# Kernel optimization log

Hardware: AMD Instinct MI355X
Metric: run time of the kernel (lower is better)

## Reference

```python
import jax, jax.numpy as jnp
import numpy as np

B, N, D, M, H = 16, 196, 512, 20, 8


def setup_inputs() -> dict:
    key = jax.random.key(0)
    ks = jax.random.split(key, 8)
    s = 0.02  # small init scale for stable activations
    return {
        "F_clean": jax.random.normal(ks[0], (B, N, D), dtype=jnp.float32),
        "in_proj_w": jax.random.normal(ks[1], (3 * D, D), dtype=jnp.float32) * s,
        "in_proj_b": jnp.zeros((3 * D,), jnp.float32),
        "out_w": jax.random.normal(ks[2], (D, D), dtype=jnp.float32) * s,
        "out_b": jnp.zeros((D,), jnp.float32),
        "w1": jax.random.normal(ks[3], (D, D), dtype=jnp.float32) * s,
        "b1": jnp.zeros((D,), jnp.float32),
        "ln_g": jnp.ones((D,), jnp.float32),
        "ln_b": jnp.zeros((D,), jnp.float32),
        "w2": jax.random.normal(ks[4], (M, D), dtype=jnp.float32) * s,
        "b2": jnp.zeros((M,), jnp.float32),
        "templates": jax.random.normal(ks[5], (M, D), dtype=jnp.float32),
        "k": 51,  # int(D * sparsity_ratio=0.1)
    }


def reference(F_clean, in_proj_w, in_proj_b, out_w, out_b, w1, b1, ln_g, ln_b, w2, b2, templates, k):
    b, n, d = F_clean.shape
    hd = d // H
    # --- MultiheadAttention (batch_first, dropout inactive at eval) ---
    qkv = F_clean @ in_proj_w.T + in_proj_b  # [B,N,3D]
    q, kk, v = jnp.split(qkv, 3, axis=-1)
    to_heads = lambda x: x.reshape(b, n, H, hd).transpose(0, 2, 1, 3)  # [B,H,N,hd]
    q, kk, v = to_heads(q), to_heads(kk), to_heads(v)
    attn = jax.nn.softmax(jnp.einsum('bhqd,bhkd->bhqk', q, kk) / jnp.sqrt(jnp.float32(hd)), axis=-1)
    o = jnp.einsum('bhqk,bhkd->bhqd', attn, v).transpose(0, 2, 1, 3).reshape(b, n, d)
    F_enh = o @ out_w.T + out_b + F_clean  # residual
    # --- decompose MLP: Linear -> LayerNorm -> GELU(exact) -> Linear ---
    h = F_enh @ w1.T + b1
    mu = h.mean(-1, keepdims=True)
    var = h.var(-1, keepdims=True)
    h = (h - mu) / jnp.sqrt(var + 1e-5) * ln_g + ln_b
    h = jax.nn.gelu(h, approximate=False)
    Qp = h @ w2.T + b2  # [B,N,M]
    # --- outer-product expansion: [B,N,D,M] ---
    Q = F_clean[:, :, :, None] * templates.T[None, None] * Qp[:, :, None, :]
    # --- per-(b,n,m) abs-topk over D, scatter 0/1 mask, L2-normalize over D ---
    A = Q.transpose(0, 1, 3, 2)  # [B,N,M,D]
    _, idx = jax.lax.top_k(jnp.abs(A), k)
    mask = jnp.put_along_axis(jnp.zeros(A.shape, A.dtype), idx, 1.0, axis=-1, inplace=False)
    Qs = A * mask
    nrm = jnp.sqrt(jnp.sum(Qs * Qs, axis=-1, keepdims=True))
    Qn = Qs / jnp.maximum(nrm, 1e-6)  # torch F.normalize clamps norm to eps
    return Qn.transpose(0, 1, 3, 2)  # [B,N,D,M]
```

## Files before the change

### kernel.cpp

```cpp
#include <hip/hip_runtime.h>
#include <cmath>


typedef __attribute__((ext_vector_type(8))) short bf16x8v;
typedef __attribute__((ext_vector_type(4))) float f32x4v;

__device__ __forceinline__ unsigned short f2bf_rne(float x) {
  unsigned u = __float_as_uint(x);
  u += 0x7fffu + ((u >> 16) & 1u);
  return (unsigned short)(u >> 16);
}
__device__ __forceinline__ float bf2f(unsigned short h) {
  return __uint_as_float(((unsigned)h) << 16);
}

__device__ __forceinline__ void split3_8(const float* xs,
    bf16x8v& o0, bf16x8v& o1, bf16x8v& o2) {
#pragma unroll
  for (int e = 0; e < 8; e++) {
    float x = xs[e];
    unsigned short s0 = f2bf_rne(x); float r1 = x - bf2f(s0);
    unsigned short s1 = f2bf_rne(r1); float r2 = r1 - bf2f(s1);
    unsigned short s2 = f2bf_rne(r2);
    o0[e] = (short)s0; o1[e] = (short)s1; o2[e] = (short)s2;
  }
}

__global__ __launch_bounds__(256) void split2_kernel(
    const float* __restrict__ X0, unsigned short* __restrict__ O0, int n0,
    const float* __restrict__ X1, unsigned short* __restrict__ O1, int n1)
{
  int nb0 = n0 >> 11;
  const float* X; unsigned short* O; long long i8, n;
  if ((int)blockIdx.x < nb0) {
    X = X0; O = O0; n = n0; i8 = (long long)blockIdx.x * 256 + threadIdx.x;
  } else {
    X = X1; O = O1; n = n1; i8 = (long long)(blockIdx.x - nb0) * 256 + threadIdx.x;
  }
  const float4 aa = *(const float4*)(X + i8 * 8);
  const float4 bb = *(const float4*)(X + i8 * 8 + 4);
  float xs[8] = {aa.x, aa.y, aa.z, aa.w, bb.x, bb.y, bb.z, bb.w};
  bf16x8v o0, o1, o2;
  split3_8(xs, o0, o1, o2);
  *(bf16x8v*)(O + i8 * 8)          = o0;
  *(bf16x8v*)(O + n + i8 * 8)      = o1;
  *(bf16x8v*)(O + 2 * n + i8 * 8)  = o2;
}

#define GBK 32
#define AROWB 80
#define SPLIT_SZ (128 * AROWB)
#define BBASE (3 * SPLIT_SZ)

__global__ __launch_bounds__(256) void gemm_ps3_kernel(
    const unsigned short* __restrict__ As, const unsigned short* __restrict__ Bs,
    float* __restrict__ C, const float* __restrict__ bias,
    const float* __restrict__ res,
    int M, int N, int ldc, long long aPlane, long long bPlane)
{
  __shared__ __align__(16) unsigned char smem[2 * BBASE];

  int tid = threadIdx.x;
  int lane = tid & 63, w = tid >> 6;
  int wrow = w >> 1, wcol = w & 1;
  int i0 = blockIdx.x * 128, j0 = blockIdx.y * 128;

  int r = tid >> 1, hh = tid & 1;
  int arow = i0 + r; if (arow > M - 1) arow = M - 1;
  int brow = j0 + r; if (brow > N - 1) brow = N - 1;
  const unsigned short* ap = As + (size_t)arow * 512 + hh * 16;
  const unsigned short* bp = Bs + (size_t)brow * 512 + hh * 16;
  unsigned swoff = (unsigned)r * AROWB + (unsigned)hh * 32;

  f32x4v acc[4][4];
#pragma unroll
  for (int fi = 0; fi < 4; fi++)
#pragma unroll
    for (int fj = 0; fj < 4; fj++) acc[fi][fj] = (f32x4v){0.f, 0.f, 0.f, 0.f};

  unsigned fr_a = (unsigned)(wrow * 64 + (lane & 15)) * AROWB + (unsigned)(lane >> 4) * 16;
  unsigned fr_b = (unsigned)(wcol * 64 + (lane & 15)) * AROWB + (unsigned)(lane >> 4) * 16 + BBASE;

  for (int k0 = 0; k0 < 512; k0 += GBK) {
    bf16x8v a0[3], a1[3], b0v[3], b1v[3];
#pragma unroll
    for (int s = 0; s < 3; s++) {
      a0[s]  = *(const bf16x8v*)(ap + s * aPlane + k0);
      a1[s]  = *(const bf16x8v*)(ap + s * aPlane + k0 + 8);
      b0v[s] = *(const bf16x8v*)(bp + s * bPlane + k0);
      b1v[s] = *(const bf16x8v*)(bp + s * bPlane + k0 + 8);
    }
    __syncthreads();
#pragma unroll
    for (int s = 0; s < 3; s++) {
      *(bf16x8v*)(smem + s * SPLIT_SZ + swoff)              = a0[s];
      *(bf16x8v*)(smem + s * SPLIT_SZ + swoff + 16)         = a1[s];
      *(bf16x8v*)(smem + BBASE + s * SPLIT_SZ + swoff)      = b0v[s];
      *(bf16x8v*)(smem + BBASE + s * SPLIT_SZ + swoff + 16) = b1v[s];
    }
    __syncthreads();

    bf16x8v af[4][3];
#pragma unroll
    for (int fi = 0; fi < 4; fi++)
#pragma unroll
      for (int s = 0; s < 3; s++)
        af[fi][s] = *(const bf16x8v*)(smem + s * SPLIT_SZ + fr_a + fi * (16 * AROWB));

#pragma unroll
    for (int fj = 0; fj < 4; fj++) {
      bf16x8v b0 = *(const bf16x8v*)(smem + 0 * SPLIT_SZ + fr_b + fj * (16 * AROWB));
      bf16x8v b1 = *(const bf16x8v*)(smem + 1 * SPLIT_SZ + fr_b + fj * (16 * AROWB));
      bf16x8v b2 = *(const bf16x8v*)(smem + 2 * SPLIT_SZ + fr_b + fj * (16 * AROWB));
#pragma unroll
      for (int fi = 0; fi < 4; fi++) {
        f32x4v c = acc[fi][fj];
        c = __builtin_amdgcn_mfma_f32_16x16x32_bf16(af[fi][2], b0, c, 0, 0, 0);
        c = __builtin_amdgcn_mfma_f32_16x16x32_bf16(af[fi][1], b1, c, 0, 0, 0);
        c = __builtin_amdgcn_mfma_f32_16x16x32_bf16(af[fi][0], b2, c, 0, 0, 0);
        c = __builtin_amdgcn_mfma_f32_16x16x32_bf16(af[fi][1], b0, c, 0, 0, 0);
        c = __builtin_amdgcn_mfma_f32_16x16x32_bf16(af[fi][0], b1, c, 0, 0, 0);
        c = __builtin_amdgcn_mfma_f32_16x16x32_bf16(af[fi][0], b0, c, 0, 0, 0);
        acc[fi][fj] = c;
      }
    }
  }

#pragma unroll
  for (int fi = 0; fi < 4; fi++) {
    int row0 = i0 + wrow * 64 + fi * 16 + (lane >> 4) * 4;
#pragma unroll
    for (int fj = 0; fj < 4; fj++) {
      int col = j0 + wcol * 64 + fj * 16 + (lane & 15);
      if (col >= N) continue;
      float badd = bias ? bias[col] : 0.0f;
      f32x4v v = acc[fi][fj];
#pragma unroll
      for (int rr = 0; rr < 4; rr++) {
        int row = row0 + rr;
        if (row < M) {
          float o = v[rr] + badd;
          if (res) o += res[(size_t)row * ldc + col];
          C[(size_t)row * ldc + col] = o;
        }
      }
    }
  }
}

__global__ __launch_bounds__(256) void gemm_bf16x3_kernel(
    const float* __restrict__ A, const float* __restrict__ B,
    float* __restrict__ C, const float* __restrict__ bias,
    const float* __restrict__ res,
    int M, int N, int K, int lda, int ldb, int ldc,
    int zInner, long long aOuter, long long aInner,
    long long bOuter, long long bInner,
    long long cOuter, long long cInner)
{
  int z = blockIdx.z;
  int zo = z / zInner, zi = z % zInner;
  A += zo * aOuter + zi * aInner;
  B += zo * bOuter + zi * bInner;
  C += zo * cOuter + zi * cInner;

  __shared__ __align__(16) unsigned char smem[2 * BBASE];

  int tid = threadIdx.x;
  int lane = tid & 63, w = tid >> 6;
  int wrow = w >> 1, wcol = w & 1;
  int i0 = blockIdx.x * 128, j0 = blockIdx.y * 128;

  int srow = tid >> 1;
  int skh  = tid & 1;
  int arow = i0 + srow; if (arow > M - 1) arow = M - 1;
  int brow = j0 + srow; if (brow > N - 1) brow = N - 1;
  const float* aptr = A + (size_t)arow * lda + skh * 16;
  const float* bptr = B + (size_t)brow * ldb + skh * 16;
  unsigned swoff = (unsigned)srow * AROWB + (unsigned)skh * 32;

  f32x4v acc[4][4];
#pragma unroll
  for (int fi = 0; fi < 4; fi++)
#pragma unroll
    for (int fj = 0; fj < 4; fj++) acc[fi][fj] = (f32x4v){0.f, 0.f, 0.f, 0.f};

  unsigned fr_a = (unsigned)(wrow * 64 + (lane & 15)) * AROWB + (unsigned)(lane >> 4) * 16;
  unsigned fr_b = (unsigned)(wcol * 64 + (lane & 15)) * AROWB + (unsigned)(lane >> 4) * 16 + BBASE;

  for (int k0 = 0; k0 < K; k0 += GBK) {
    float av[16], bv[16];
    {
      const float4 q0 = *(const float4*)(aptr + k0);
      const float4 q1 = *(const float4*)(aptr + k0 + 4);
      const float4 q2 = *(const float4*)(aptr + k0 + 8);
      const float4 q3 = *(const float4*)(aptr + k0 + 12);
      av[0]=q0.x; av[1]=q0.y; av[2]=q0.z; av[3]=q0.w;
      av[4]=q1.x; av[5]=q1.y; av[6]=q1.z; av[7]=q1.w;
      av[8]=q2.x; av[9]=q2.y; av[10]=q2.z; av[11]=q2.w;
      av[12]=q3.x; av[13]=q3.y; av[14]=q3.z; av[15]=q3.w;
      const float4 r0 = *(const float4*)(bptr + k0);
      const float4 r1 = *(const float4*)(bptr + k0 + 4);
      const float4 r2 = *(const float4*)(bptr + k0 + 8);
      const float4 r3 = *(const float4*)(bptr + k0 + 12);
      bv[0]=r0.x; bv[1]=r0.y; bv[2]=r0.z; bv[3]=r0.w;
      bv[4]=r1.x; bv[5]=r1.y; bv[6]=r1.z; bv[7]=r1.w;
      bv[8]=r2.x; bv[9]=r2.y; bv[10]=r2.z; bv[11]=r2.w;
      bv[12]=r3.x; bv[13]=r3.y; bv[14]=r3.z; bv[15]=r3.w;
    }
    unsigned short ha[3][16], hb[3][16];
#pragma unroll
    for (int e = 0; e < 16; e++) {
      float x = av[e];
      unsigned short s0 = f2bf_rne(x); float r = x - bf2f(s0);
      unsigned short s1 = f2bf_rne(r); float r2 = r - bf2f(s1);
      unsigned short s2 = f2bf_rne(r2);
      ha[0][e] = s0; ha[1][e] = s1; ha[2][e] = s2;
      float y = bv[e];
      unsigned short t0 = f2bf_rne(y); float u = y - bf2f(t0);
      unsigned short t1 = f2bf_rne(u); float u2 = u - bf2f(t1);
      unsigned short t2 = f2bf_rne(u2);
      hb[0][e] = t0; hb[1][e] = t1; hb[2][e] = t2;
    }
    __syncthreads();
#pragma unroll
    for (int s = 0; s < 3; s++) {
      bf16x8v v0, v1, w0, w1;
#pragma unroll
      for (int e = 0; e < 8; e++) {
        v0[e] = (short)ha[s][e]; v1[e] = (short)ha[s][8 + e];
        w0[e] = (short)hb[s][e]; w1[e] = (short)hb[s][8 + e];
      }
      *(bf16x8v*)(smem + s * SPLIT_SZ + swoff)              = v0;
      *(bf16x8v*)(smem + s * SPLIT_SZ + swoff + 16)         = v1;
      *(bf16x8v*)(smem + BBASE + s * SPLIT_SZ + swoff)      = w0;
      *(bf16x8v*)(smem + BBASE + s * SPLIT_SZ + swoff + 16) = w1;
    }
    __syncthreads();

    bf16x8v af[4][3];
#pragma unroll
    for (int fi = 0; fi < 4; fi++)
#pragma unroll
      for (int s = 0; s < 3; s++)
        af[fi][s] = *(const bf16x8v*)(smem + s * SPLIT_SZ + fr_a + fi * (16 * AROWB));

#pragma unroll
    for (int fj = 0; fj < 4; fj++) {
      bf16x8v b0 = *(const bf16x8v*)(smem + 0 * SPLIT_SZ + fr_b + fj * (16 * AROWB));
      bf16x8v b1 = *(const bf16x8v*)(smem + 1 * SPLIT_SZ + fr_b + fj * (16 * AROWB));
      bf16x8v b2 = *(const bf16x8v*)(smem + 2 * SPLIT_SZ + fr_b + fj * (16 * AROWB));
#pragma unroll
      for (int fi = 0; fi < 4; fi++) {
        f32x4v c = acc[fi][fj];
        c = __builtin_amdgcn_mfma_f32_16x16x32_bf16(af[fi][2], b0, c, 0, 0, 0);
        c = __builtin_amdgcn_mfma_f32_16x16x32_bf16(af[fi][1], b1, c, 0, 0, 0);
        c = __builtin_amdgcn_mfma_f32_16x16x32_bf16(af[fi][0], b2, c, 0, 0, 0);
        c = __builtin_amdgcn_mfma_f32_16x16x32_bf16(af[fi][1], b0, c, 0, 0, 0);
        c = __builtin_amdgcn_mfma_f32_16x16x32_bf16(af[fi][0], b1, c, 0, 0, 0);
        c = __builtin_amdgcn_mfma_f32_16x16x32_bf16(af[fi][0], b0, c, 0, 0, 0);
        acc[fi][fj] = c;
      }
    }
  }

#pragma unroll
  for (int fi = 0; fi < 4; fi++) {
    int row0 = i0 + wrow * 64 + fi * 16 + (lane >> 4) * 4;
#pragma unroll
    for (int fj = 0; fj < 4; fj++) {
      int col = j0 + wcol * 64 + fj * 16 + (lane & 15);
      if (col >= N) continue;
      float badd = bias ? bias[col] : 0.0f;
      f32x4v v = acc[fi][fj];
#pragma unroll
      for (int rr = 0; rr < 4; rr++) {
        int row = row0 + rr;
        if (row < M) {
          float o = v[rr] + badd;
          if (res) o += res[(size_t)row * ldc + col];
          C[(size_t)row * ldc + col] = o;
        }
      }
    }
  }
}

__global__ __launch_bounds__(256) void vtrans_kernel(
    const float* __restrict__ qkv, float* __restrict__ Vt)
{
  __shared__ float lds[224 * 65];
  int z = blockIdx.x;
  int b = z >> 3, h = z & 7;
  int tid = threadIdx.x;
  const float* src = qkv + ((size_t)b * 196) * 1536 + 1024 + h * 64;
  for (int idx = tid; idx < 224 * 64; idx += 256) {
    int kk = idx >> 6, d = idx & 63;
    lds[kk * 65 + d] = (kk < 196) ? src[(size_t)kk * 1536 + d] : 0.0f;
  }
  __syncthreads();
  float* dst = Vt + (size_t)z * (64 * 224);
  for (int idx = tid; idx < 64 * 224; idx += 256) {
    int d = idx / 224, kk = idx - d * 224;
    dst[idx] = lds[kk * 65 + d];
  }
}

__global__ __launch_bounds__(256) void softmax_kernel(float* __restrict__ S)
{
  int row = blockIdx.x * 4 + (threadIdx.x >> 6);
  int lane = threadIdx.x & 63;
  float* sr = S + (size_t)row * 196;
  double v[4];
#pragma unroll
  for (int t = 0; t < 4; t++) {
    int j = lane + 64 * t;
    v[t] = (j < 196) ? (double)sr[j] * 0.125 : -1e300;
  }
  double mx = fmax(fmax(v[0], v[1]), fmax(v[2], v[3]));
#pragma unroll
  for (int off = 1; off < 64; off <<= 1) mx = fmax(mx, __shfl_xor(mx, off));
  double e[4]; double s = 0.0;
#pragma unroll
  for (int t = 0; t < 4; t++) {
    int j = lane + 64 * t;
    e[t] = (j < 196) ? exp(v[t] - mx) : 0.0;
    s += e[t];
  }
#pragma unroll
  for (int off = 1; off < 64; off <<= 1) s += __shfl_xor(s, off);
  double inv = 1.0 / s;
#pragma unroll
  for (int t = 0; t < 4; t++) {
    int j = lane + 64 * t;
    if (j < 196) sr[j] = (float)(e[t] * inv);
  }
}

__global__ __launch_bounds__(256) void lngelu_kernel(float* __restrict__ H,
    const float* __restrict__ g, const float* __restrict__ bb)
{
  int row = blockIdx.x;
  float* hr = H + (size_t)row * 512;
  int tid = threadIdx.x, lane = tid & 63, wv = tid >> 6;
  __shared__ double red[8];
  double x0 = (double)hr[tid], x1 = (double)hr[tid + 256];
  double s = x0 + x1;
#pragma unroll
  for (int off = 1; off < 64; off <<= 1) s += __shfl_xor(s, off);
  if (lane == 0) red[wv] = s;
  __syncthreads();
  double mu = (red[0] + red[1] + red[2] + red[3]) * (1.0 / 512.0);
  double d0 = x0 - mu, d1 = x1 - mu;
  double q = d0 * d0 + d1 * d1;
#pragma unroll
  for (int off = 1; off < 64; off <<= 1) q += __shfl_xor(q, off);
  if (lane == 0) red[4 + wv] = q;
  __syncthreads();
  double var = (red[4] + red[5] + red[6] + red[7]) * (1.0 / 512.0);
  double inv = 1.0 / sqrt(var + 1e-5);
  double y0 = d0 * inv * (double)g[tid]       + (double)bb[tid];
  double y1 = d1 * inv * (double)g[tid + 256] + (double)bb[tid + 256];
  const double ISQRT2 = 0.70710678118654752440;
  double z0 = 0.5 * y0 * (1.0 + erf(y0 * ISQRT2));
  double z1 = 0.5 * y1 * (1.0 + erf(y1 * ISQRT2));
  hr[tid] = (float)z0;
  hr[tid + 256] = (float)z1;
}

__global__ __launch_bounds__(256) void w2_kernel(const float* __restrict__ H,
    const float* __restrict__ W2, const float* __restrict__ B2,
    float* __restrict__ Qp)
{
  int gidx = blockIdx.x * 256 + threadIdx.x;
  int token = gidx / 20, m = gidx % 20;
  const float* hr = H + (size_t)token * 512;
  const float* wr = W2 + (size_t)m * 512;
  double acc = 0.0;
  for (int k = 0; k < 512; k += 4) {
    float4 hv = *(const float4*)&hr[k];
    float4 wv = *(const float4*)&wr[k];
    acc += (double)hv.x * wv.x + (double)hv.y * wv.y +
           (double)hv.z * wv.z + (double)hv.w * wv.w;
  }
  Qp[gidx] = (float)(acc + (double)B2[m]);
}

__global__ __launch_bounds__(256) void topk_select_kernel(
    const float* __restrict__ F, const float* __restrict__ T,
    const float* __restrict__ Qp, unsigned long long* __restrict__ masks,
    float* __restrict__ qif)
{
  const int KSEL = 51;
  int g = blockIdx.x * 4 + (threadIdx.x >> 6);
  int lane = threadIdx.x & 63;
  int bn = g / 20, m = g - bn * 20;
  const float* Frow = F + (size_t)bn * 512;
  const float* Trow = T + (size_t)m * 512;

  unsigned uh[8], ul[8];
  float apf[8];
#pragma unroll
  for (int s = 0; s < 8; s++) {
    double p = (double)Frow[lane + 64 * s] * (double)Trow[lane + 64 * s];
    unsigned long long u =
        (unsigned long long)__double_as_longlong(p) & 0x7fffffffffffffffULL;
    uh[s] = (unsigned)(u >> 32);
    ul[s] = (unsigned)u;
    apf[s] = (float)fabs(p);
  }

  unsigned mx = 0u, mn = 0xffffffffu;
#pragma unroll
  for (int s = 0; s < 8; s++) {
    mx = uh[s] > mx ? uh[s] : mx;
    mn = uh[s] < mn ? uh[s] : mn;
  }
#pragma unroll
  for (int off = 1; off < 64; off <<= 1) {
    unsigned omx = __shfl_xor(mx, off);
    unsigned omn = __shfl_xor(mn, off);
    mx = omx > mx ? omx : mx;
    mn = omn < mn ? omn : mn;
  }

  unsigned lo = mn, hi = mx + 1u;
  bool exact = false;
  while (hi - lo > 1u) {
    unsigned mid = lo + ((hi - lo) >> 1);
    int c = 0;
#pragma unroll
    for (int s = 0; s < 8; s++) c += (int)__popcll(__ballot(uh[s] >= mid));
    if (c >= KSEL) { lo = mid; if (c == KSEL) { exact = true; break; } }
    else hi = mid;
  }
  unsigned thrh = lo;

  bool sel[8];
  if (exact) {
#pragma unroll
    for (int s = 0; s < 8; s++) sel[s] = (uh[s] >= thrh);
  } else {
    int cg = 0;
#pragma unroll
    for (int s = 0; s < 8; s++) {
      sel[s] = (uh[s] > thrh);
      cg += (int)__popcll(__ballot(sel[s]));
    }
    int need = KSEL - cg;
    bool tk[8];
#pragma unroll
    for (int s = 0; s < 8; s++) tk[s] = false;
    while (need > 0) {
      unsigned long long bk = 0ULL;
#pragma unroll
      for (int s = 0; s < 8; s++) {
        if (uh[s] == thrh && !tk[s]) {
          unsigned long long key = (1ULL << 41)
                                 | ((unsigned long long)ul[s] << 9)
                                 | ((unsigned long long)(7 - s) << 6)
                                 | (unsigned long long)(63 - lane);
          bk = key > bk ? key : bk;
        }
      }
#pragma unroll
      for (int off = 1; off < 64; off <<= 1) {
        unsigned long long ob = __shfl_xor(bk, off);
        bk = ob > bk ? ob : bk;
      }
      if ((int)(63 - (bk & 63ULL)) == lane) {
        int ws = 7 - (int)((bk >> 6) & 7ULL);
        sel[ws] = true;
        tk[ws] = true;
      }
      need--;
    }
  }

  float ss = 0.f;
  unsigned long long selb[8];
#pragma unroll
  for (int s = 0; s < 8; s++) {
    selb[s] = __ballot((int)sel[s]);
    if (sel[s]) ss += apf[s] * apf[s];
  }
#pragma unroll
  for (int off = 1; off < 64; off <<= 1) ss += __shfl_xor(ss, off);
  float qp = Qp[g];
  float nrm = fabsf(qp) * sqrtf(ss);
  float qid = qp / fmaxf(nrm, 1e-6f);
  if (lane == 0) {
    qif[g] = qid;
#pragma unroll
    for (int s = 0; s < 8; s++) masks[(size_t)g * 8 + s] = selb[s];
  }
}

__global__ __launch_bounds__(256) void topk_write_kernel(
    const float* __restrict__ F, const float* __restrict__ T,
    const unsigned long long* __restrict__ masks,
    const float* __restrict__ qif, float* __restrict__ out)
{
  int bn = blockIdx.x;
  int tid = threadIdx.x;
  __shared__ unsigned long long mw[20][8];
  __shared__ float qf[20];
  __shared__ float vt[256][21];
  if (tid < 160) ((unsigned long long*)mw)[tid] = masks[(size_t)bn * 160 + tid];
  if (tid < 20) qf[tid] = qif[(size_t)bn * 20 + tid];
  const float* Frow = F + (size_t)bn * 512;
  float* orow = out + (size_t)bn * 10240;
  __syncthreads();

#pragma unroll
  for (int half = 0; half < 2; half++) {
    int d = half * 256 + tid;
    float fd = Frow[d];
    int dw = d >> 6, db = d & 63;
#pragma unroll
    for (int m = 0; m < 20; m++) {
      bool sel = (mw[m][dw] >> db) & 1ULL;
      float tv = T[(size_t)m * 512 + d];
      vt[tid][m] = sel ? fd * tv * qf[m] : 0.0f;
    }
    __syncthreads();
#pragma unroll
    for (int k = 0; k < 5; k++) {
      int flat = (k * 256 + tid) * 4;
      float v[4];
#pragma unroll
      for (int e = 0; e < 4; e++) {
        int fe = flat + e;
        int dl = fe / 20;
        int mm = fe - dl * 20;
        v[e] = vt[dl][mm];
      }
      float4 o = {v[0], v[1], v[2], v[3]};
      *(float4*)&orow[half * 5120 + flat] = o;
    }
    __syncthreads();
  }
}

extern "C" void kernel_launch(void* const* d_in, const int* in_sizes, int n_in,
                              void* d_out, int out_size, void* d_ws, size_t ws_size,
                              hipStream_t stream) {
  const float* F    = (const float*)d_in[0];
  const float* Wqkv = (const float*)d_in[1];
  const float* bqkv = (const float*)d_in[2];
  const float* Wo   = (const float*)d_in[3];
  const float* bo   = (const float*)d_in[4];
  const float* W1   = (const float*)d_in[5];
  const float* b1   = (const float*)d_in[6];
  const float* lng  = (const float*)d_in[7];
  const float* lnb  = (const float*)d_in[8];
  const float* W2   = (const float*)d_in[9];
  const float* b2   = (const float*)d_in[10];
  const float* Tm   = (const float*)d_in[11];
  float* out = (float*)d_out;

  float* ws     = (float*)d_ws;
  float* qkv    = ws;
  float* scores = ws + 4816896;
  float* Omg    = ws + 9734144;
  float* Fenh   = ws + 11339776;
  float* h1     = ws + 12945408;
  float* Qp     = ws + 14551040;
  float* Vt = Fenh;
  unsigned short* Fs    = (unsigned short*)scores;
  unsigned short* Wqkvs = (unsigned short*)(scores + 2408448);
  unsigned short* Omgs  = (unsigned short*)scores;
  unsigned short* Wos   = (unsigned short*)(scores + 2408448);
  unsigned short* Fenhs = (unsigned short*)qkv;
  unsigned short* W1s   = (unsigned short*)(qkv + 2408448);
  unsigned long long* masks = (unsigned long long*)qkv;
  float* qifb = (float*)(masks + (size_t)62720 * 8);
  dim3 blk(256);

  split2_kernel<<<dim3(1168), blk, 0, stream>>>(
      F, Fs, 1605632, Wqkv, Wqkvs, 786432);

  gemm_ps3_kernel<<<dim3(25, 12), blk, 0, stream>>>(
      Fs, Wqkvs, qkv, bqkv, nullptr, 3136, 1536, 1536, 1605632LL, 786432LL);

  vtrans_kernel<<<dim3(128), blk, 0, stream>>>(qkv, Vt);

  gemm_bf16x3_kernel<<<dim3(2, 2, 128), blk, 0, stream>>>(
      qkv, qkv + 512, scores, nullptr, nullptr,
      196, 196, 64, 1536, 1536, 196,
      8, 196LL * 1536, 64, 196LL * 1536, 64, 8LL * 38416, 38416);

  softmax_kernel<<<dim3(6272), blk, 0, stream>>>(scores);

  gemm_bf16x3_kernel<<<dim3(2, 1, 128), blk, 0, stream>>>(
      scores, Vt, Omg, nullptr, nullptr,
      196, 64, 196, 196, 224, 512,
      8, 8LL * 38416, 38416, 8LL * 14336, 14336, 100352, 64);

  split2_kernel<<<dim3(912), blk, 0, stream>>>(
      Omg, Omgs, 1605632, Wo, Wos, 262144);

  gemm_ps3_kernel<<<dim3(25, 4), blk, 0, stream>>>(
      Omgs, Wos, Fenh, bo, F, 3136, 512, 512, 1605632LL, 262144LL);

  split2_kernel<<<dim3(912), blk, 0, stream>>>(
      Fenh, Fenhs, 1605632, W1, W1s, 262144);

  gemm_ps3_kernel<<<dim3(25, 4), blk, 0, stream>>>(
      Fenhs, W1s, h1, b1, nullptr, 3136, 512, 512, 1605632LL, 262144LL);

  lngelu_kernel<<<dim3(3136), blk, 0, stream>>>(h1, lng, lnb);

  w2_kernel<<<dim3(245), blk, 0, stream>>>(h1, W2, b2, Qp);

  topk_select_kernel<<<dim3(15680), blk, 0, stream>>>(F, Tm, Qp, masks, qifb);

  topk_write_kernel<<<dim3(3136), blk, 0, stream>>>(F, Tm, masks, qifb, out);
}
```

Measured before the change: 372.9 us.

## Fuse bf16 splits into GEMM epilogues, merge LN+W2, pair topk rows per wave

Weight splits for Wo and W1 move into the first split launch. The attention-output and out-proj GEMMs now write their results directly as three bf16 planes in the epilogue, which removes two standalone split kernels and their fp32 intermediate round trips. LayerNorm+GELU is fused with the W2 projection in one per-row kernel that keeps the activations in LDS. Top-k selection processes two templates per wave, sharing the F load and interleaving both binary searches. Costs are strided scalar 2-byte epilogue stores, extra register pressure in topk, and a new workspace layout.

```diff
diff --git a/kernel.cpp b/kernel.cpp
--- a/kernel.cpp
+++ b/kernel.cpp
@@ -13,30 +13,35 @@
 __device__ __forceinline__ float bf2f(unsigned short h) {
   return __uint_as_float(((unsigned)h) << 16);
 }
-
+__device__ __forceinline__ void split3_1(float x,
+    unsigned short& s0, unsigned short& s1, unsigned short& s2) {
+  s0 = f2bf_rne(x); float r1 = x - bf2f(s0);
+  s1 = f2bf_rne(r1); float r2 = r1 - bf2f(s1);
+  s2 = f2bf_rne(r2);
+}
 __device__ __forceinline__ void split3_8(const float* xs,
     bf16x8v& o0, bf16x8v& o1, bf16x8v& o2) {
 #pragma unroll
   for (int e = 0; e < 8; e++) {
-    float x = xs[e];
-    unsigned short s0 = f2bf_rne(x); float r1 = x - bf2f(s0);
-    unsigned short s1 = f2bf_rne(r1); float r2 = r1 - bf2f(s1);
-    unsigned short s2 = f2bf_rne(r2);
-    o0[e] = (short)s0; o1[e] = (short)s1; o2[e] = (short)s2;
-  }
-}
-
-__global__ __launch_bounds__(256) void split2_kernel(
+    unsigned short a, b, c;
+    split3_1(xs[e], a, b, c);
+    o0[e] = (short)a; o1[e] = (short)b; o2[e] = (short)c;
+  }
+}
+
+__global__ __launch_bounds__(256) void split4_kernel(
     const float* __restrict__ X0, unsigned short* __restrict__ O0, int n0,
-    const float* __restrict__ X1, unsigned short* __restrict__ O1, int n1)
-{
-  int nb0 = n0 >> 11;
+    const float* __restrict__ X1, unsigned short* __restrict__ O1, int n1,
+    const float* __restrict__ X2, unsigned short* __restrict__ O2, int n2,
+    const float* __restrict__ X3, unsigned short* __restrict__ O3, int n3)
+{
+  int nb0 = n0 >> 11, nb1 = n1 >> 11, nb2 = n2 >> 11;
+  int b = blockIdx.x;
   const float* X; unsigned short* O; long long i8, n;
-  if ((int)blockIdx.x < nb0) {
-    X = X0; O = O0; n = n0; i8 = (long long)blockIdx.x * 256 + threadIdx.x;
-  } else {
-    X = X1; O = O1; n = n1; i8 = (long long)(blockIdx.x - nb0) * 256 + threadIdx.x;
-  }
+  if (b < nb0)                   { X = X0; O = O0; n = n0; i8 = (long long)b * 256 + threadIdx.x; }
+  else if (b < nb0 + nb1)        { X = X1; O = O1; n = n1; i8 = (long long)(b - nb0) * 256 + threadIdx.x; }
+  else if (b < nb0 + nb1 + nb2)  { X = X2; O = O2; n = n2; i8 = (long long)(b - nb0 - nb1) * 256 + threadIdx.x; }
+  else                           { X = X3; O = O3; n = n3; i8 = (long long)(b - nb0 - nb1 - nb2) * 256 + threadIdx.x; }
   const float4 aa = *(const float4*)(X + i8 * 8);
   const float4 bb = *(const float4*)(X + i8 * 8 + 4);
   float xs[8] = {aa.x, aa.y, aa.z, aa.w, bb.x, bb.y, bb.z, bb.w};
@@ -56,7 +61,8 @@
     const unsigned short* __restrict__ As, const unsigned short* __restrict__ Bs,
     float* __restrict__ C, const float* __restrict__ bias,
     const float* __restrict__ res,
-    int M, int N, int ldc, long long aPlane, long long bPlane)
+    int M, int N, int ldc, long long aPlane, long long bPlane,
+    unsigned short* __restrict__ Cl, long long clPlane)
 {
   __shared__ __align__(16) unsigned char smem[2 * BBASE];
 
@@ -141,7 +147,14 @@
         if (row < M) {
           float o = v[rr] + badd;
           if (res) o += res[(size_t)row * ldc + col];
-          C[(size_t)row * ldc + col] = o;
+          size_t idx = (size_t)row * ldc + col;
+          if (Cl) {
+            unsigned short l0, l1, l2;
+            split3_1(o, l0, l1, l2);
+            Cl[idx] = l0; Cl[idx + clPlane] = l1; Cl[idx + 2 * clPlane] = l2;
+          } else {
+            C[idx] = o;
+          }
         }
       }
     }
@@ -155,13 +168,16 @@
     int M, int N, int K, int lda, int ldb, int ldc,
     int zInner, long long aOuter, long long aInner,
     long long bOuter, long long bInner,
-    long long cOuter, long long cInner)
+    long long cOuter, long long cInner,
+    unsigned short* __restrict__ Cl, long long clPlane)
 {
   int z = blockIdx.z;
   int zo = z / zInner, zi = z % zInner;
   A += zo * aOuter + zi * aInner;
   B += zo * bOuter + zi * bInner;
-  C += zo * cOuter + zi * cInner;
+  long long coff = zo * cOuter + zi * cInner;
+  if (C) C += coff;
+  if (Cl) Cl += coff;
 
   __shared__ __align__(16) unsigned char smem[2 * BBASE];
 
@@ -210,16 +226,8 @@
     unsigned short ha[3][16], hb[3][16];
 #pragma unroll
     for (int e = 0; e < 16; e++) {
-      float x = av[e];
-      unsigned short s0 = f2bf_rne(x); float r = x - bf2f(s0);
-      unsigned short s1 = f2bf_rne(r); float r2 = r - bf2f(s1);
-      unsigned short s2 = f2bf_rne(r2);
-      ha[0][e] = s0; ha[1][e] = s1; ha[2][e] = s2;
-      float y = bv[e];
-      unsigned short t0 = f2bf_rne(y); float u = y - bf2f(t0);
-      unsigned short t1 = f2bf_rne(u); float u2 = u - bf2f(t1);
-      unsigned short t2 = f2bf_rne(u2);
-      hb[0][e] = t0; hb[1][e] = t1; hb[2][e] = t2;
+      split3_1(av[e], ha[0][e], ha[1][e], ha[2][e]);
+      split3_1(bv[e], hb[0][e], hb[1][e], hb[2][e]);
     }
     __syncthreads();
 #pragma unroll
@@ -278,7 +286,14 @@
         if (row < M) {
           float o = v[rr] + badd;
           if (res) o += res[(size_t)row * ldc + col];
-          C[(size_t)row * ldc + col] = o;
+          size_t idx = (size_t)row * ldc + col;
+          if (Cl) {
+            unsigned short l0, l1, l2;
+            split3_1(o, l0, l1, l2);
+            Cl[idx] = l0; Cl[idx + clPlane] = l1; Cl[idx + 2 * clPlane] = l2;
+          } else {
+            C[idx] = o;
+          }
         }
       }
     }
@@ -336,13 +351,16 @@
   }
 }
 
-__global__ __launch_bounds__(256) void lngelu_kernel(float* __restrict__ H,
-    const float* __restrict__ g, const float* __restrict__ bb)
+__global__ __launch_bounds__(256) void lnw2_kernel(
+    const float* __restrict__ H, const float* __restrict__ g,
+    const float* __restrict__ bb, const float* __restrict__ W2,
+    const float* __restrict__ B2, float* __restrict__ Qp)
 {
   int row = blockIdx.x;
-  float* hr = H + (size_t)row * 512;
+  const float* hr = H + (size_t)row * 512;
   int tid = threadIdx.x, lane = tid & 63, wv = tid >> 6;
   __shared__ double red[8];
+  __shared__ float y[512];
   double x0 = (double)hr[tid], x1 = (double)hr[tid + 256];
   double s = x0 + x1;
 #pragma unroll
@@ -363,78 +381,32 @@
   const double ISQRT2 = 0.70710678118654752440;
   double z0 = 0.5 * y0 * (1.0 + erf(y0 * ISQRT2));
   double z1 = 0.5 * y1 * (1.0 + erf(y1 * ISQRT2));
-  hr[tid] = (float)z0;
-  hr[tid + 256] = (float)z1;
-}
-
-__global__ __launch_bounds__(256) void w2_kernel(const float* __restrict__ H,
-    const float* __restrict__ W2, const float* __restrict__ B2,
-    float* __restrict__ Qp)
-{
-  int gidx = blockIdx.x * 256 + threadIdx.x;
-  int token = gidx / 20, m = gidx % 20;
-  const float* hr = H + (size_t)token * 512;
-  const float* wr = W2 + (size_t)m * 512;
-  double acc = 0.0;
-  for (int k = 0; k < 512; k += 4) {
-    float4 hv = *(const float4*)&hr[k];
-    float4 wv = *(const float4*)&wr[k];
-    acc += (double)hv.x * wv.x + (double)hv.y * wv.y +
-           (double)hv.z * wv.z + (double)hv.w * wv.w;
-  }
-  Qp[gidx] = (float)(acc + (double)B2[m]);
-}
-
-__global__ __launch_bounds__(256) void topk_select_kernel(
-    const float* __restrict__ F, const float* __restrict__ T,
-    const float* __restrict__ Qp, unsigned long long* __restrict__ masks,
-    float* __restrict__ qif)
+  y[tid] = (float)z0;
+  y[tid + 256] = (float)z1;
+  __syncthreads();
+
+#pragma unroll 1
+  for (int t = 0; t < 5; t++) {
+    int m = wv * 5 + t;
+    const float* wr = W2 + (size_t)m * 512;
+    double acc = 0.0;
+#pragma unroll
+    for (int sE = 0; sE < 8; sE++) {
+      int j = lane + 64 * sE;
+      acc += (double)y[j] * (double)wr[j];
+    }
+#pragma unroll
+    for (int off = 1; off < 64; off <<= 1) acc += __shfl_xor(acc, off);
+    if (lane == 0) Qp[(size_t)row * 20 + m] = (float)(acc + (double)B2[m]);
+  }
+}
+
+__device__ __forceinline__ void topk_finish32(
+    const unsigned* uh, const unsigned* ul, const float* apf,
+    unsigned thrh, bool exact, float qp, int g,
+    unsigned long long* __restrict__ masks, float* __restrict__ qif, int lane)
 {
   const int KSEL = 51;
-  int g = blockIdx.x * 4 + (threadIdx.x >> 6);
-  int lane = threadIdx.x & 63;
-  int bn = g / 20, m = g - bn * 20;
-  const float* Frow = F + (size_t)bn * 512;
-  const float* Trow = T + (size_t)m * 512;
-
-  unsigned uh[8], ul[8];
-  float apf[8];
-#pragma unroll
-  for (int s = 0; s < 8; s++) {
-    double p = (double)Frow[lane + 64 * s] * (double)Trow[lane + 64 * s];
-    unsigned long long u =
-        (unsigned long long)__double_as_longlong(p) & 0x7fffffffffffffffULL;
-    uh[s] = (unsigned)(u >> 32);
-    ul[s] = (unsigned)u;
-    apf[s] = (float)fabs(p);
-  }
-
-  unsigned mx = 0u, mn = 0xffffffffu;
-#pragma unroll
-  for (int s = 0; s < 8; s++) {
-    mx = uh[s] > mx ? uh[s] : mx;
-    mn = uh[s] < mn ? uh[s] : mn;
-  }
-#pragma unroll
-  for (int off = 1; off < 64; off <<= 1) {
-    unsigned omx = __shfl_xor(mx, off);
-    unsigned omn = __shfl_xor(mn, off);
-    mx = omx > mx ? omx : mx;
-    mn = omn < mn ? omn : mn;
-  }
-
-  unsigned lo = mn, hi = mx + 1u;
-  bool exact = false;
-  while (hi - lo > 1u) {
-    unsigned mid = lo + ((hi - lo) >> 1);
-    int c = 0;
-#pragma unroll
-    for (int s = 0; s < 8; s++) c += (int)__popcll(__ballot(uh[s] >= mid));
-    if (c >= KSEL) { lo = mid; if (c == KSEL) { exact = true; break; } }
-    else hi = mid;
-  }
-  unsigned thrh = lo;
-
   bool sel[8];
   if (exact) {
 #pragma unroll
@@ -468,9 +440,9 @@
         bk = ob > bk ? ob : bk;
       }
       if ((int)(63 - (bk & 63ULL)) == lane) {
-        int ws = 7 - (int)((bk >> 6) & 7ULL);
-        sel[ws] = true;
-        tk[ws] = true;
+        int wsI = 7 - (int)((bk >> 6) & 7ULL);
+        sel[wsI] = true;
+        tk[wsI] = true;
       }
       need--;
     }
@@ -485,7 +457,6 @@
   }
 #pragma unroll
   for (int off = 1; off < 64; off <<= 1) ss += __shfl_xor(ss, off);
-  float qp = Qp[g];
   float nrm = fabsf(qp) * sqrtf(ss);
   float qid = qp / fmaxf(nrm, 1e-6f);
   if (lane == 0) {
@@ -493,6 +464,77 @@
 #pragma unroll
     for (int s = 0; s < 8; s++) masks[(size_t)g * 8 + s] = selb[s];
   }
+}
+
+__global__ __launch_bounds__(256) void topk_select_kernel(
+    const float* __restrict__ F, const float* __restrict__ T,
+    const float* __restrict__ Qp, unsigned long long* __restrict__ masks,
+    float* __restrict__ qif)
+{
+  const int KSEL = 51;
+  int wid = blockIdx.x * 4 + (threadIdx.x >> 6);
+  int lane = threadIdx.x & 63;
+  int g0 = wid * 2;
+  int bn = g0 / 20, m0 = g0 - bn * 20;
+  const float* Frow = F + (size_t)bn * 512;
+  const float* T0r = T + (size_t)m0 * 512;
+  const float* T1r = T0r + 512;
+
+  unsigned uh0[8], ul0[8], uh1[8], ul1[8];
+  float ap0[8], ap1[8];
+#pragma unroll
+  for (int s = 0; s < 8; s++) {
+    double fd = (double)Frow[lane + 64 * s];
+    double p0 = fd * (double)T0r[lane + 64 * s];
+    double p1 = fd * (double)T1r[lane + 64 * s];
+    unsigned long long u0 =
+        (unsigned long long)__double_as_longlong(p0) & 0x7fffffffffffffffULL;
+    unsigned long long u1 =
+        (unsigned long long)__double_as_longlong(p1) & 0x7fffffffffffffffULL;
+    uh0[s] = (unsigned)(u0 >> 32); ul0[s] = (unsigned)u0;
+    uh1[s] = (unsigned)(u1 >> 32); ul1[s] = (unsigned)u1;
+    ap0[s] = (float)fabs(p0); ap1[s] = (float)fabs(p1);
+  }
+
+  unsigned mx0 = 0u, mn0 = 0xffffffffu, mx1 = 0u, mn1 = 0xffffffffu;
+#pragma unroll
+  for (int s = 0; s < 8; s++) {
+    mx0 = uh0[s] > mx0 ? uh0[s] : mx0;  mn0 = uh0[s] < mn0 ? uh0[s] : mn0;
+    mx1 = uh1[s] > mx1 ? uh1[s] : mx1;  mn1 = uh1[s] < mn1 ? uh1[s] : mn1;
+  }
+#pragma unroll
+  for (int off = 1; off < 64; off <<= 1) {
+    unsigned a = __shfl_xor(mx0, off); mx0 = a > mx0 ? a : mx0;
+    unsigned b = __shfl_xor(mn0, off); mn0 = b < mn0 ? b : mn0;
+    unsigned c = __shfl_xor(mx1, off); mx1 = c > mx1 ? c : mx1;
+    unsigned d = __shfl_xor(mn1, off); mn1 = d < mn1 ? d : mn1;
+  }
+
+  unsigned lo0 = mn0, hi0 = mx0 + 1u, lo1 = mn1, hi1 = mx1 + 1u;
+  bool ex0 = false, ex1 = false;
+  bool dn0 = (hi0 - lo0 <= 1u), dn1 = (hi1 - lo1 <= 1u);
+  while (!(dn0 && dn1)) {
+    if (!dn0) {
+      unsigned mid = lo0 + ((hi0 - lo0) >> 1);
+      int c = 0;
+#pragma unroll
+      for (int s = 0; s < 8; s++) c += (int)__popcll(__ballot(uh0[s] >= mid));
+      if (c >= KSEL) { lo0 = mid; if (c == KSEL) { ex0 = true; dn0 = true; } }
+      else hi0 = mid;
+      dn0 = dn0 || (hi0 - lo0 <= 1u);
+    }
+    if (!dn1) {
+      unsigned mid = lo1 + ((hi1 - lo1) >> 1);
+      int c = 0;
+#pragma unroll
+      for (int s = 0; s < 8; s++) c += (int)__popcll(__ballot(uh1[s] >= mid));
+      if (c >= KSEL) { lo1 = mid; if (c == KSEL) { ex1 = true; dn1 = true; } }
+      else hi1 = mid;
+      dn1 = dn1 || (hi1 - lo1 <= 1u);
+    }
+  }
+  topk_finish32(uh0, ul0, ap0, lo0, ex0, Qp[g0],     g0,     masks, qif, lane);
+  topk_finish32(uh1, ul1, ap1, lo1, ex1, Qp[g0 + 1], g0 + 1, masks, qif, lane);
 }
 
 __global__ __launch_bounds__(256) void topk_write_kernel(
@@ -561,58 +603,54 @@
   float* ws     = (float*)d_ws;
   float* qkv    = ws;
   float* scores = ws + 4816896;
-  float* Omg    = ws + 9734144;
-  float* Fenh   = ws + 11339776;
-  float* h1     = ws + 12945408;
-  float* Qp     = ws + 14551040;
-  float* Vt = Fenh;
+  float* Vt     = ws + 9734144;
+  float* h1     = ws + 11569152;
+  float* Qp     = ws + 13174784;
+  unsigned short* Wos   = (unsigned short*)(ws + 13237504);
+  unsigned short* W1s   = (unsigned short*)(ws + 13630720);
+  unsigned short* Omgs  = (unsigned short*)(ws + 14023936);
+  unsigned short* Fenhs = (unsigned short*)(ws + 16432384);
   unsigned short* Fs    = (unsigned short*)scores;
   unsigned short* Wqkvs = (unsigned short*)(scores + 2408448);
-  unsigned short* Omgs  = (unsigned short*)scores;
-  unsigned short* Wos   = (unsigned short*)(scores + 2408448);
-  unsigned short* Fenhs = (unsigned short*)qkv;
-  unsigned short* W1s   = (unsigned short*)(qkv + 2408448);
   unsigned long long* masks = (unsigned long long*)qkv;
   float* qifb = (float*)(masks + (size_t)62720 * 8);
   dim3 blk(256);
 
-  split2_kernel<<<dim3(1168), blk, 0, stream>>>(
-      F, Fs, 1605632, Wqkv, Wqkvs, 786432);
+  split4_kernel<<<dim3(1424), blk, 0, stream>>>(
+      F, Fs, 1605632, Wqkv, Wqkvs, 786432,
+      Wo, Wos, 262144, W1, W1s, 262144);
 
   gemm_ps3_kernel<<<dim3(25, 12), blk, 0, stream>>>(
-      Fs, Wqkvs, qkv, bqkv, nullptr, 3136, 1536, 1536, 1605632LL, 786432LL);
+      Fs, Wqkvs, qkv, bqkv, nullptr, 3136, 1536, 1536, 1605632LL, 786432LL,
+      nullptr, 0);
 
   vtrans_kernel<<<dim3(128), blk, 0, stream>>>(qkv, Vt);
 
   gemm_bf16x3_kernel<<<dim3(2, 2, 128), blk, 0, stream>>>(
       qkv, qkv + 512, scores, nullptr, nullptr,
       196, 196, 64, 1536, 1536, 196,
-      8, 196LL * 1536, 64, 196LL * 1536, 64, 8LL * 38416, 38416);
+      8, 196LL * 1536, 64, 196LL * 1536, 64, 8LL * 38416, 38416,
+      nullptr, 0);
 
   softmax_kernel<<<dim3(6272), blk, 0, stream>>>(scores);
 
   gemm_bf16x3_kernel<<<dim3(2, 1, 128), blk, 0, stream>>>(
-      scores, Vt, Omg, nullptr, nullptr,
+      scores, Vt, nullptr, nullptr, nullptr,
       196, 64, 196, 196, 224, 512,
-      8, 8LL * 38416, 38416, 8LL * 14336, 14336, 100352, 64);
-
-  split2_kernel<<<dim3(912), blk, 0, stream>>>(
-      Omg, Omgs, 1605632, Wo, Wos, 262144);
+      8, 8LL * 38416, 38416, 8LL * 14336, 14336, 100352, 64,
+      Omgs, 1605632LL);
 
   gemm_ps3_kernel<<<dim3(25, 4), blk, 0, stream>>>(
-      Omgs, Wos, Fenh, bo, F, 3136, 512, 512, 1605632LL, 262144LL);
-
-  split2_kernel<<<dim3(912), blk, 0, stream>>>(
-      Fenh, Fenhs, 1605632, W1, W1s, 262144);
+      Omgs, Wos, nullptr, bo, F, 3136, 512, 512, 1605632LL, 262144LL,
+      Fenhs, 1605632LL);
 
   gemm_ps3_kernel<<<dim3(25, 4), blk, 0, stream>>>(
-      Fenhs, W1s, h1, b1, nullptr, 3136, 512, 512, 1605632LL, 262144LL);
-
-  lngelu_kernel<<<dim3(3136), blk, 0, stream>>>(h1, lng, lnb);
-
-  w2_kernel<<<dim3(245), blk, 0, stream>>>(h1, W2, b2, Qp);
-
-  topk_select_kernel<<<dim3(15680), blk, 0, stream>>>(F, Tm, Qp, masks, qifb);
+      Fenhs, W1s, h1, b1, nullptr, 3136, 512, 512, 1605632LL, 262144LL,
+      nullptr, 0);
+
+  lnw2_kernel<<<dim3(3136), blk, 0, stream>>>(h1, lng, lnb, W2, b2, Qp);
+
+  topk_select_kernel<<<dim3(7840), blk, 0, stream>>>(F, Tm, Qp, masks, qifb);
 
   topk_write_kernel<<<dim3(3136), blk, 0, stream>>>(F, Tm, masks, qifb, out);
 }
```

After: 370.1 us. Within noise of the previous version (-0.8%).
